# Optimization experiments

Measured on AMD Instinct MI355X. Metric: run time of the kernel, lower is better.

## Reference

```python
import jax, jax.numpy as jnp
import numpy as np

N_WAY, N_SHOT, C, H, W = 5, 5, 640, 32, 32
EPS = 1e-12


def conv1x1(x, w, b):
    # 1x1 conv == channel GEMM; w: (C_out, C_in), b: (C_out,)
    return jnp.einsum('bchw,oc->bohw', x, w) + b[None, :, None, None]


def setup_inputs() -> dict:
    key = jax.random.key(0)
    ks = jax.random.split(key, 7)
    B = N_WAY * N_SHOT
    x5 = jax.random.normal(ks[0], (B, C, H, W), jnp.float32)
    Wc = jax.random.normal(ks[1], (C, C), jnp.float32) * 0.02
    bc = jax.random.normal(ks[2], (C,), jnp.float32) * 0.02
    Wq = jax.random.normal(ks[3], (C, C), jnp.float32) * 0.02
    bq = jax.random.normal(ks[4], (C,), jnp.float32) * 0.02
    Wk = jax.random.normal(ks[5], (C, C), jnp.float32) * 0.02
    bk = jax.random.normal(ks[6], (C,), jnp.float32) * 0.02
    return {"x5": x5, "Wc": Wc, "bc": bc, "Wq": Wq, "bq": bq, "Wk": Wk, "bk": bk}


def reference(x5, Wc, bc, Wq, bq, Wk, bk):
    B, Cc, Hh, Ww = x5.shape
    HW = Hh * Ww
    scale = 1.0 / (Cc ** 0.5)

    # residual 1x1 conv, then query_transform applied once (x5 is reassigned)
    x5 = conv1x1(x5, Wc, bc) + x5
    x5 = conv1x1(x5, Wq, bq)

    # query: query_transform applied AGAIN on the already-transformed x5
    xq = conv1x1(x5, Wq, bq).reshape(N_WAY, N_SHOT, Cc, HW)
    xq = xq.transpose(0, 1, 3, 2).reshape(N_WAY, N_SHOT * HW, Cc)
    xk = conv1x1(x5, Wk, bk).reshape(N_WAY, N_SHOT, Cc, HW)
    xk = xk.transpose(0, 2, 1, 3).reshape(N_WAY, Cc, N_SHOT * HW)

    # QK scores per way: (n_way, S*HW, S*HW)
    xw = jnp.matmul(xq, xk) * scale
    # max over key spatial, mean over key shot
    xw = xw.reshape(N_WAY, N_SHOT * HW, N_SHOT, HW).max(-1).mean(-1)
    xw = jax.nn.softmax(xw.reshape(N_WAY, N_SHOT, HW), axis=-1)

    # channel-wise L2 normalize (F.normalize semantics)
    nrm = jnp.maximum(jnp.sqrt((x5 * x5).sum(1, keepdims=True)), EPS)
    norm0 = (x5 / nrm).reshape(N_WAY, N_SHOT, Cc, Hh, Ww)

    # argmax-equality mask over spatial positions
    xw_max = xw.max(-1, keepdims=True)
    mask = (xw == xw_max).astype(x5.dtype).reshape(N_WAY, N_SHOT, 1, Hh, Ww)

    # seeds: masked spatial sum of normalized features -> (n_way, n_shot, C)
    seeds = (norm0 * mask).sum((3, 4))

    # conv3d correlation: out[b,o,h,w] = sum_{k,c} norm0[b,k,c,h,w] * seeds[o,k,c]
    cm = jnp.einsum('bkchw,okc->bohw', norm0, seeds).reshape(N_WAY, N_WAY, HW)
    cmin = cm.min(-1, keepdims=True)
    cmax = cm.max(-1, keepdims=True)
    cm = (cm - cmin) / (cmax - cmin + EPS)
    cormap = cm.reshape(B, 1, Hh, Ww)

    x51 = (x5 * cormap).reshape(N_WAY, N_SHOT, Cc, Hh, Ww)
    proto1 = x51.mean((1, 3, 4))  # (n_way, C)
    return proto1
```

## Files before the change

kernel.cpp:

```cpp
#include <hip/hip_runtime.h>
#include <math.h>

#define NW 5
#define NS 5
#define CDIM 640
#define HWDIM 1024
#define BDIM 25
constexpr int CHW = CDIM * HWDIM;
constexpr int NBIG = BDIM * CHW;
constexpr int WSZ = CDIM * CDIM;
constexpr float QK_SCALE = 0.03952847075210474f;

typedef __attribute__((ext_vector_type(4))) float f32x4;
typedef __attribute__((ext_vector_type(8))) __bf16 bf16x8;
typedef __attribute__((ext_vector_type(4))) __bf16 bf16x4;
typedef __attribute__((ext_vector_type(2))) __bf16 bf16x2;

__device__ __forceinline__ void load_lds16(const __bf16* g, __bf16* l) {
    __builtin_amdgcn_global_load_lds(
        (const __attribute__((address_space(1))) void*)g,
        (__attribute__((address_space(3))) void*)l, 16, 0, 0);
}

__global__ __launch_bounds__(256) void split_f32(const float* __restrict__ s,
                                                 __bf16* __restrict__ dH,
                                                 __bf16* __restrict__ dL, int n4) {
    int i = blockIdx.x * 256 + threadIdx.x;
    if (i >= n4) return;
    f32x4 v = reinterpret_cast<const f32x4*>(s)[i];
    bf16x4 h, lo;
    #pragma unroll
    for (int q = 0; q < 4; ++q) {
        __bf16 hh = (__bf16)v[q];
        h[q] = hh;
        lo[q] = (__bf16)(v[q] - (float)hh);
    }
    reinterpret_cast<bf16x4*>(dH)[i] = h;
    reinterpret_cast<bf16x4*>(dL)[i] = lo;
}

__global__ __launch_bounds__(256) void tsplit(const float* __restrict__ x,
                                              __bf16* __restrict__ dH,
                                              __bf16* __restrict__ dL) {
    __shared__ float sT[32][33];
    const int hw0 = blockIdx.x * 32, c0 = blockIdx.y * 32, b = blockIdx.z;
    const int t = threadIdx.x;
    const int r = t >> 3, q4 = (t & 7) * 4;
    f32x4 v = *reinterpret_cast<const f32x4*>(
        &x[(size_t)b * CHW + (size_t)(c0 + r) * HWDIM + hw0 + q4]);
    #pragma unroll
    for (int i = 0; i < 4; ++i) sT[r][q4 + i] = v[i];
    __syncthreads();
    bf16x4 h, lo;
    #pragma unroll
    for (int i = 0; i < 4; ++i) {
        float xv = sT[q4 + i][r];
        __bf16 hh = (__bf16)xv;
        h[i] = hh;
        lo[i] = (__bf16)(xv - (float)hh);
    }
    size_t off = (size_t)b * CHW + (size_t)(hw0 + r) * CDIM + c0 + q4;
    *reinterpret_cast<bf16x4*>(&dH[off]) = h;
    *reinterpret_cast<bf16x4*>(&dL[off]) = lo;
}

template <int RES>
__global__ __launch_bounds__(256) void conv_mfma(
    const __bf16* __restrict__ inH, const __bf16* __restrict__ inL,
    const __bf16* __restrict__ wH, const __bf16* __restrict__ wL,
    const float* __restrict__ bias,
    __bf16* __restrict__ outH, __bf16* __restrict__ outL) {
    __shared__ __bf16 sA[2][128][32];
    __shared__ __bf16 sB[2][128][32];
    const int hw0 = blockIdx.x * 128;
    const int o0 = blockIdx.y * 128;
    const int b = blockIdx.z;
    const int tid = threadIdx.x;
    const int wv = tid >> 6, l = tid & 63;
    const int wo = (wv >> 1) * 64, wh = (wv & 1) * 64;
    const size_t inBase = (size_t)b * CHW;

    f32x4 acc[4][4];
    #pragma unroll
    for (int i = 0; i < 4; ++i)
        #pragma unroll
        for (int j = 0; j < 4; ++j) acc[i][j] = (f32x4){0.f, 0.f, 0.f, 0.f};

    const int srow = l >> 2;
    const int scol = (l & 3) * 8;
    const int fr = l & 15, fo = (l >> 4) * 8;

    for (int c0 = 0; c0 < CDIM; c0 += 32) {
        #pragma unroll
        for (int i = 0; i < 2; ++i) {
            const int r = wv * 32 + i * 16;
            const int gr = r + srow;
            load_lds16(&wH[(size_t)(o0 + gr) * CDIM + c0 + scol], &sA[0][r][0]);
            load_lds16(&wL[(size_t)(o0 + gr) * CDIM + c0 + scol], &sA[1][r][0]);
            load_lds16(&inH[inBase + (size_t)(hw0 + gr) * CDIM + c0 + scol],
                       &sB[0][r][0]);
            load_lds16(&inL[inBase + (size_t)(hw0 + gr) * CDIM + c0 + scol],
                       &sB[1][r][0]);
        }
        __syncthreads();
        bf16x8 aH[4], aL[4], bH[4], bL[4];
        #pragma unroll
        for (int i = 0; i < 4; ++i) {
            aH[i] = *reinterpret_cast<const bf16x8*>(&sA[0][wo + i * 16 + fr][fo]);
            aL[i] = *reinterpret_cast<const bf16x8*>(&sA[1][wo + i * 16 + fr][fo]);
            bH[i] = *reinterpret_cast<const bf16x8*>(&sB[0][wh + i * 16 + fr][fo]);
            bL[i] = *reinterpret_cast<const bf16x8*>(&sB[1][wh + i * 16 + fr][fo]);
        }
        #pragma unroll
        for (int i = 0; i < 4; ++i)
            #pragma unroll
            for (int j = 0; j < 4; ++j) {
                acc[i][j] = __builtin_amdgcn_mfma_f32_16x16x32_bf16(
                    aH[i], bH[j], acc[i][j], 0, 0, 0);
                acc[i][j] = __builtin_amdgcn_mfma_f32_16x16x32_bf16(
                    aH[i], bL[j], acc[i][j], 0, 0, 0);
                acc[i][j] = __builtin_amdgcn_mfma_f32_16x16x32_bf16(
                    aL[i], bH[j], acc[i][j], 0, 0, 0);
            }
        __syncthreads();
    }

    const int og = (l >> 4) * 4;
    const int cl = l & 15;
    #pragma unroll
    for (int i = 0; i < 4; ++i) {
        const int o = o0 + wo + i * 16 + og;
        const f32x4 bs = *reinterpret_cast<const f32x4*>(&bias[o]);
        #pragma unroll
        for (int j = 0; j < 4; ++j) {
            const int hw = hw0 + wh + j * 16 + cl;
            const size_t off = inBase + (size_t)hw * CDIM + o;
            float r[4];
            #pragma unroll
            for (int q = 0; q < 4; ++q) r[q] = acc[i][j][q] + bs[q];
            if (RES) {
                bf16x4 rh = *reinterpret_cast<const bf16x4*>(&inH[off]);
                bf16x4 rl = *reinterpret_cast<const bf16x4*>(&inL[off]);
                #pragma unroll
                for (int q = 0; q < 4; ++q) r[q] += (float)rh[q] + (float)rl[q];
            }
            bf16x4 oh, ol;
            #pragma unroll
            for (int q = 0; q < 4; ++q) {
                __bf16 hh = (__bf16)r[q];
                oh[q] = hh;
                ol[q] = (__bf16)(r[q] - (float)hh);
            }
            *reinterpret_cast<bf16x4*>(&outH[off]) = oh;
            *reinterpret_cast<bf16x4*>(&outL[off]) = ol;
        }
    }
}

__global__ __launch_bounds__(256) void attn_mfma(
    const __bf16* __restrict__ qH, const __bf16* __restrict__ qL,
    const __bf16* __restrict__ kH, const __bf16* __restrict__ kL,
    float* __restrict__ gpart) {
    __shared__ __bf16 sQ[2][128][32];
    __shared__ __bf16 sK[2][128][32];
    __shared__ float sRed[2][128];
    const int qt = blockIdx.x;
    const int ks = blockIdx.y, wy = blockIdx.z;
    const int sq = qt >> 3, q0 = (qt & 7) * 128;
    const int tid = threadIdx.x;
    const int wv = tid >> 6, l = tid & 63;
    const int wq = (wv >> 1) * 64;
    const int kh = wv & 1;
    const int wk = kh * 64;
    const size_t qBase = (size_t)(wy * NS + sq) * CHW;
    const size_t kBase = (size_t)(wy * NS + ks) * CHW;

    float qmax[4][4];
    #pragma unroll
    for (int i = 0; i < 4; ++i)
        #pragma unroll
        for (int q = 0; q < 4; ++q) qmax[i][q] = -INFINITY;

    const int srow = l >> 2, scol = (l & 3) * 8;
    const int fr = l & 15, fo = (l >> 4) * 8;

    for (int kc = 0; kc < HWDIM; kc += 128) {
        f32x4 acc[4][4];
        #pragma unroll
        for (int i = 0; i < 4; ++i)
            #pragma unroll
            for (int j = 0; j < 4; ++j) acc[i][j] = (f32x4){0.f, 0.f, 0.f, 0.f};

        for (int c0 = 0; c0 < CDIM; c0 += 32) {
            #pragma unroll
            for (int i = 0; i < 2; ++i) {
                const int r = wv * 32 + i * 16;
                const int gr = r + srow;
                load_lds16(&qH[qBase + (size_t)(q0 + gr) * CDIM + c0 + scol],
                           &sQ[0][r][0]);
                load_lds16(&qL[qBase + (size_t)(q0 + gr) * CDIM + c0 + scol],
                           &sQ[1][r][0]);
                load_lds16(&kH[kBase + (size_t)(kc + gr) * CDIM + c0 + scol],
                           &sK[0][r][0]);
                load_lds16(&kL[kBase + (size_t)(kc + gr) * CDIM + c0 + scol],
                           &sK[1][r][0]);
            }
            __syncthreads();
            bf16x8 aH[4], aL[4], bH[4], bL[4];
            #pragma unroll
            for (int i = 0; i < 4; ++i) {
                aH[i] = *reinterpret_cast<const bf16x8*>(&sQ[0][wq + i * 16 + fr][fo]);
                aL[i] = *reinterpret_cast<const bf16x8*>(&sQ[1][wq + i * 16 + fr][fo]);
                bH[i] = *reinterpret_cast<const bf16x8*>(&sK[0][wk + i * 16 + fr][fo]);
                bL[i] = *reinterpret_cast<const bf16x8*>(&sK[1][wk + i * 16 + fr][fo]);
            }
            #pragma unroll
            for (int i = 0; i < 4; ++i)
                #pragma unroll
                for (int j = 0; j < 4; ++j) {
                    acc[i][j] = __builtin_amdgcn_mfma_f32_16x16x32_bf16(
                        aH[i], bH[j], acc[i][j], 0, 0, 0);
                    acc[i][j] = __builtin_amdgcn_mfma_f32_16x16x32_bf16(
                        aH[i], bL[j], acc[i][j], 0, 0, 0);
                    acc[i][j] = __builtin_amdgcn_mfma_f32_16x16x32_bf16(
                        aL[i], bH[j], acc[i][j], 0, 0, 0);
                }
            __syncthreads();
        }
        #pragma unroll
        for (int i = 0; i < 4; ++i)
            #pragma unroll
            for (int q = 0; q < 4; ++q) {
                float m = fmaxf(fmaxf(acc[i][0][q], acc[i][1][q]),
                                fmaxf(acc[i][2][q], acc[i][3][q]));
                qmax[i][q] = fmaxf(qmax[i][q], m);
            }
    }
    #pragma unroll
    for (int i = 0; i < 4; ++i)
        #pragma unroll
        for (int q = 0; q < 4; ++q) {
            float v = qmax[i][q];
            v = fmaxf(v, __shfl_xor(v, 1));
            v = fmaxf(v, __shfl_xor(v, 2));
            v = fmaxf(v, __shfl_xor(v, 4));
            v = fmaxf(v, __shfl_xor(v, 8));
            qmax[i][q] = v;
        }
    if ((l & 15) == 0) {
        const int g = l >> 4;
        #pragma unroll
        for (int i = 0; i < 4; ++i)
            #pragma unroll
            for (int q = 0; q < 4; ++q)
                sRed[kh][wq + i * 16 + g * 4 + q] = qmax[i][q];
    }
    __syncthreads();
    if (tid < 128) {
        float m = fmaxf(sRed[0][tid], sRed[1][tid]);
        gpart[(size_t)(wy * NS + ks) * (NS * HWDIM) + sq * HWDIM + q0 + tid] =
            m * QK_SCALE;
    }
}

__global__ __launch_bounds__(256) void softmax_mask(const float* __restrict__ gpart,
                                                    int* __restrict__ gIdx,
                                                    int* __restrict__ gCnt) {
    const int bb = blockIdx.x;
    const int w = bb / NS, sq = bb % NS;
    const int tid = threadIdx.x;
    __shared__ float sred[256];
    __shared__ int sCnt;

    float v[4];
    #pragma unroll
    for (int i = 0; i < 4; ++i) {
        int hw = tid + 256 * i;
        float s = 0.f;
        #pragma unroll
        for (int ks = 0; ks < NS; ++ks)
            s += gpart[(size_t)(w * NS + ks) * (NS * HWDIM) + sq * HWDIM + hw];
        v[i] = s * 0.2f;
    }
    float m = fmaxf(fmaxf(v[0], v[1]), fmaxf(v[2], v[3]));
    sred[tid] = m;
    __syncthreads();
    for (int s = 128; s > 0; s >>= 1) {
        if (tid < s) sred[tid] = fmaxf(sred[tid], sred[tid + s]);
        __syncthreads();
    }
    float rowmax = sred[0];
    __syncthreads();
    float e[4], ls = 0.f;
    #pragma unroll
    for (int i = 0; i < 4; ++i) { e[i] = expf(v[i] - rowmax); ls += e[i]; }
    sred[tid] = ls;
    __syncthreads();
    for (int s = 128; s > 0; s >>= 1) {
        if (tid < s) sred[tid] += sred[tid + s];
        __syncthreads();
    }
    float ssum = sred[0];
    __syncthreads();
    float p[4], pm = 0.f;
    #pragma unroll
    for (int i = 0; i < 4; ++i) { p[i] = e[i] / ssum; pm = fmaxf(pm, p[i]); }
    sred[tid] = pm;
    __syncthreads();
    for (int s = 128; s > 0; s >>= 1) {
        if (tid < s) sred[tid] = fmaxf(sred[tid], sred[tid + s]);
        __syncthreads();
    }
    float pmax = sred[0];
    if (tid == 0) sCnt = 0;
    __syncthreads();
    #pragma unroll
    for (int i = 0; i < 4; ++i) {
        if (p[i] == pmax) {
            int slot = atomicAdd(&sCnt, 1);
            gIdx[bb * HWDIM + slot] = tid + 256 * i;
        }
    }
    __syncthreads();
    if (tid == 0) gCnt[bb] = sCnt;
}

__global__ __launch_bounds__(256) void nrm_k(const __bf16* __restrict__ yH,
                                             const __bf16* __restrict__ yL,
                                             float* __restrict__ inv) {
    const int row = blockIdx.x * 16 + (threadIdx.x >> 4);
    const int cq = threadIdx.x & 15;
    const size_t base = (size_t)row * CDIM;
    float s = 0.f;
    #pragma unroll
    for (int i = 0; i < 10; ++i) {
        int c = i * 64 + cq * 4;
        bf16x4 h = *reinterpret_cast<const bf16x4*>(&yH[base + c]);
        bf16x4 lo = *reinterpret_cast<const bf16x4*>(&yL[base + c]);
        #pragma unroll
        for (int q = 0; q < 4; ++q) {
            float x = (float)h[q] + (float)lo[q];
            s = fmaf(x, x, s);
        }
    }
    s += __shfl_xor(s, 1);
    s += __shfl_xor(s, 2);
    s += __shfl_xor(s, 4);
    s += __shfl_xor(s, 8);
    if (cq == 0) inv[row] = 1.0f / fmaxf(sqrtf(s), 1e-12f);
}

__global__ __launch_bounds__(640) void seeds_k(const __bf16* __restrict__ yH,
                                               const __bf16* __restrict__ yL,
                                               const float* __restrict__ inv,
                                               const int* __restrict__ gIdx,
                                               const int* __restrict__ gCnt,
                                               float* __restrict__ seeds) {
    const int bb = blockIdx.x, c = threadIdx.x;
    const int cnt = gCnt[bb];
    float s = 0.f;
    for (int e = 0; e < cnt; ++e) {
        int hw = gIdx[bb * HWDIM + e];
        size_t off = (size_t)bb * CHW + (size_t)hw * CDIM + c;
        s += ((float)yH[off] + (float)yL[off]) * inv[bb * HWDIM + hw];
    }
    seeds[bb * CDIM + c] = s;
}

__global__ __launch_bounds__(256) void cm_k(const __bf16* __restrict__ yH,
                                            const __bf16* __restrict__ yL,
                                            const float* __restrict__ inv,
                                            const float* __restrict__ seeds,
                                            float* __restrict__ cm) {
    __shared__ float sS[BDIM * CDIM];
    const int way = blockIdx.y;
    const int tid = threadIdx.x, wv = tid >> 6, l = tid & 63;
    const int hw = blockIdx.x * 4 + wv;
    for (int e = tid; e < BDIM * CDIM; e += 256) sS[e] = seeds[e];
    __syncthreads();
    float acc[NW] = {0.f, 0.f, 0.f, 0.f, 0.f};
    for (int k = 0; k < NS; ++k) {
        const size_t base = (size_t)(way * NS + k) * CHW + (size_t)hw * CDIM;
        float t[NW] = {0.f, 0.f, 0.f, 0.f, 0.f};
        #pragma unroll
        for (int i = 0; i < 5; ++i) {
            int c = (i * 64 + l) * 2;
            bf16x2 h = *reinterpret_cast<const bf16x2*>(&yH[base + c]);
            bf16x2 lo = *reinterpret_cast<const bf16x2*>(&yL[base + c]);
            float x0 = (float)h[0] + (float)lo[0];
            float x1 = (float)h[1] + (float)lo[1];
            #pragma unroll
            for (int o = 0; o < NW; ++o) {
                t[o] = fmaf(x0, sS[(o * NS + k) * CDIM + c], t[o]);
                t[o] = fmaf(x1, sS[(o * NS + k) * CDIM + c + 1], t[o]);
            }
        }
        float iv = inv[(way * NS + k) * HWDIM + hw];
        #pragma unroll
        for (int o = 0; o < NW; ++o) acc[o] = fmaf(t[o], iv, acc[o]);
    }
    #pragma unroll
    for (int o = 0; o < NW; ++o) {
        float v = acc[o];
        v += __shfl_xor(v, 1);
        v += __shfl_xor(v, 2);
        v += __shfl_xor(v, 4);
        v += __shfl_xor(v, 8);
        v += __shfl_xor(v, 16);
        v += __shfl_xor(v, 32);
        if (l == 0) cm[(size_t)(way * NW + o) * HWDIM + hw] = v;
    }
}

__global__ __launch_bounds__(256) void minmax_kernel(float* __restrict__ cm) {
    const int row = blockIdx.x;
    const int tid = threadIdx.x;
    __shared__ float smn[256], smx[256];
    float v[4];
    #pragma unroll
    for (int i = 0; i < 4; ++i) v[i] = cm[(size_t)row * HWDIM + tid + 256 * i];
    float mn = fminf(fminf(v[0], v[1]), fminf(v[2], v[3]));
    float mx = fmaxf(fmaxf(v[0], v[1]), fmaxf(v[2], v[3]));
    smn[tid] = mn;
    smx[tid] = mx;
    __syncthreads();
    for (int s = 128; s > 0; s >>= 1) {
        if (tid < s) {
            smn[tid] = fminf(smn[tid], smn[tid + s]);
            smx[tid] = fmaxf(smx[tid], smx[tid + s]);
        }
        __syncthreads();
    }
    float cmin = smn[0], cmax = smx[0];
    float den = cmax - cmin + 1e-12f;
    #pragma unroll
    for (int i = 0; i < 4; ++i)
        cm[(size_t)row * HWDIM + tid + 256 * i] = (v[i] - cmin) / den;
}

__global__ __launch_bounds__(128) void proto_part_k(const __bf16* __restrict__ yH,
                                                    const __bf16* __restrict__ yL,
                                                    const float* __restrict__ cmn,
                                                    float* __restrict__ part) {
    const int w = blockIdx.x, cc = blockIdx.y, hs = blockIdx.z;
    const int c = cc * 128 + threadIdx.x;
    float s = 0.f;
    for (int i = 0; i < 640; ++i) {
        int g = hs * 640 + i, sh = g >> 10, hw = g & 1023;
        size_t off = (size_t)(w * NS + sh) * CHW + (size_t)hw * CDIM + c;
        s = fmaf((float)yH[off] + (float)yL[off],
                 cmn[(w * NS + sh) * HWDIM + hw], s);
    }
    part[((w * 5 + cc) * 8 + hs) * 128 + threadIdx.x] = s;
}

__global__ __launch_bounds__(128) void proto_red_k(const float* __restrict__ part,
                                                   float* __restrict__ out) {
    const int bid = blockIdx.x;
    float s = 0.f;
    #pragma unroll
    for (int hs = 0; hs < 8; ++hs) s += part[(bid * 8 + hs) * 128 + threadIdx.x];
    const int w = bid / 5, cc = bid % 5;
    out[w * CDIM + cc * 128 + threadIdx.x] = s * (1.0f / 5120.0f);
}

extern "C" void kernel_launch(void* const* d_in, const int* in_sizes, int n_in,
                              void* d_out, int out_size, void* d_ws, size_t ws_size,
                              hipStream_t stream) {
    const float* x5 = (const float*)d_in[0];
    const float* Wc = (const float*)d_in[1];
    const float* bc = (const float*)d_in[2];
    const float* Wq = (const float*)d_in[3];
    const float* bq = (const float*)d_in[4];
    const float* Wk = (const float*)d_in[5];
    const float* bk = (const float*)d_in[6];
    float* out = (float*)d_out;

    __bf16* big = (__bf16*)d_ws;
    __bf16* A_hi = big;
    __bf16* A_lo = big + (size_t)NBIG;
    __bf16* B_hi = big + (size_t)2 * NBIG;
    __bf16* B_lo = big + (size_t)3 * NBIG;
    __bf16* C_hi = big + (size_t)4 * NBIG;
    __bf16* C_lo = big + (size_t)5 * NBIG;
    __bf16* wp = big + (size_t)6 * NBIG;
    __bf16* WcH = wp;
    __bf16* WcL = wp + WSZ;
    __bf16* WqH = wp + 2 * WSZ;
    __bf16* WqL = wp + 3 * WSZ;
    __bf16* WkH = wp + 4 * WSZ;
    __bf16* WkL = wp + 5 * WSZ;
    float* fp = (float*)(wp + 6 * WSZ);
    float* gpart = fp;
    float* invb = fp + 128000;
    float* seedsb = fp + 153600;
    float* cmb = fp + 169600;
    float* partb = fp + 195200;
    int* gIdx = (int*)(fp + 220800);
    int* gCnt = gIdx + BDIM * HWDIM;

    const int W4 = WSZ / 4;
    split_f32<<<dim3((W4 + 255) / 256), 256, 0, stream>>>(Wc, WcH, WcL, W4);
    split_f32<<<dim3((W4 + 255) / 256), 256, 0, stream>>>(Wq, WqH, WqL, W4);
    split_f32<<<dim3((W4 + 255) / 256), 256, 0, stream>>>(Wk, WkH, WkL, W4);
    tsplit<<<dim3(32, 20, 25), 256, 0, stream>>>(x5, A_hi, A_lo);

    dim3 gG(8, 5, 25);
    conv_mfma<1><<<gG, 256, 0, stream>>>(A_hi, A_lo, WcH, WcL, bc, B_hi, B_lo);
    conv_mfma<0><<<gG, 256, 0, stream>>>(B_hi, B_lo, WqH, WqL, bq, C_hi, C_lo);
    conv_mfma<0><<<gG, 256, 0, stream>>>(C_hi, C_lo, WqH, WqL, bq, B_hi, B_lo);
    conv_mfma<0><<<gG, 256, 0, stream>>>(C_hi, C_lo, WkH, WkL, bk, A_hi, A_lo);

    attn_mfma<<<dim3(40, 5, 5), 256, 0, stream>>>(B_hi, B_lo, A_hi, A_lo, gpart);
    softmax_mask<<<25, 256, 0, stream>>>(gpart, gIdx, gCnt);
    nrm_k<<<1600, 256, 0, stream>>>(C_hi, C_lo, invb);
    seeds_k<<<25, 640, 0, stream>>>(C_hi, C_lo, invb, gIdx, gCnt, seedsb);
    cm_k<<<dim3(256, 5), 256, 0, stream>>>(C_hi, C_lo, invb, seedsb, cmb);
    minmax_kernel<<<25, 256, 0, stream>>>(cmb);
    proto_part_k<<<dim3(5, 5, 8), 128, 0, stream>>>(C_hi, C_lo, cmb, partb);
    proto_red_k<<<25, 128, 0, stream>>>(partb, out);
}
```

Baseline: 1.072 ms.

## Interleave hi/lo bf16 tiles in XOR-swizzled LDS rows and raise MFMA priority

```diff
diff --git a/kernel.cpp b/kernel.cpp
--- a/kernel.cpp
+++ b/kernel.cpp
@@ -64,14 +64,29 @@
     *reinterpret_cast<bf16x4*>(&dL[off]) = lo;
 }
 
+
+__device__ __forceinline__ void stage_tile(const __bf16* __restrict__ srcH,
+                                           const __bf16* __restrict__ srcL,
+                                           __bf16* lds, int wv, int l, int c0) {
+    const int lch = (l & 7) ^ (l >> 3);
+    const int scol = (lch & 3) * 8;
+    const int srw = l >> 3;
+    const __bf16* src = (lch & 4) ? srcL : srcH;
+    #pragma unroll
+    for (int i = 0; i < 4; ++i) {
+        const int r0 = wv * 32 + i * 8;
+        load_lds16(&src[(size_t)(r0 + srw) * CDIM + c0 + scol], &lds[r0 * 64]);
+    }
+}
+
 template <int RES>
 __global__ __launch_bounds__(256) void conv_mfma(
     const __bf16* __restrict__ inH, const __bf16* __restrict__ inL,
     const __bf16* __restrict__ wH, const __bf16* __restrict__ wL,
     const float* __restrict__ bias,
     __bf16* __restrict__ outH, __bf16* __restrict__ outL) {
-    __shared__ __bf16 sA[2][128][32];
-    __shared__ __bf16 sB[2][128][32];
+    __shared__ __bf16 sA[128 * 64];
+    __shared__ __bf16 sB[128 * 64];
     const int hw0 = blockIdx.x * 128;
     const int o0 = blockIdx.y * 128;
     const int b = blockIdx.z;
@@ -80,36 +95,33 @@
     const int wo = (wv >> 1) * 64, wh = (wv & 1) * 64;
     const size_t inBase = (size_t)b * CHW;
 
+    const __bf16* wSrcH = wH + (size_t)o0 * CDIM;
+    const __bf16* wSrcL = wL + (size_t)o0 * CDIM;
+    const __bf16* iSrcH = inH + inBase + (size_t)hw0 * CDIM;
+    const __bf16* iSrcL = inL + inBase + (size_t)hw0 * CDIM;
+
     f32x4 acc[4][4];
     #pragma unroll
     for (int i = 0; i < 4; ++i)
         #pragma unroll
         for (int j = 0; j < 4; ++j) acc[i][j] = (f32x4){0.f, 0.f, 0.f, 0.f};
 
-    const int srow = l >> 2;
-    const int scol = (l & 3) * 8;
-    const int fr = l & 15, fo = (l >> 4) * 8;
+    const int fr = l & 15, cf = l >> 4;
+    const int ehi = (cf ^ (fr & 7)) * 8;
 
     for (int c0 = 0; c0 < CDIM; c0 += 32) {
-        #pragma unroll
-        for (int i = 0; i < 2; ++i) {
-            const int r = wv * 32 + i * 16;
-            const int gr = r + srow;
-            load_lds16(&wH[(size_t)(o0 + gr) * CDIM + c0 + scol], &sA[0][r][0]);
-            load_lds16(&wL[(size_t)(o0 + gr) * CDIM + c0 + scol], &sA[1][r][0]);
-            load_lds16(&inH[inBase + (size_t)(hw0 + gr) * CDIM + c0 + scol],
-                       &sB[0][r][0]);
-            load_lds16(&inL[inBase + (size_t)(hw0 + gr) * CDIM + c0 + scol],
-                       &sB[1][r][0]);
-        }
+        stage_tile(wSrcH, wSrcL, sA, wv, l, c0);
+        stage_tile(iSrcH, iSrcL, sB, wv, l, c0);
         __syncthreads();
         bf16x8 aH[4], aL[4], bH[4], bL[4];
         #pragma unroll
         for (int i = 0; i < 4; ++i) {
-            aH[i] = *reinterpret_cast<const bf16x8*>(&sA[0][wo + i * 16 + fr][fo]);
-            aL[i] = *reinterpret_cast<const bf16x8*>(&sA[1][wo + i * 16 + fr][fo]);
-            bH[i] = *reinterpret_cast<const bf16x8*>(&sB[0][wh + i * 16 + fr][fo]);
-            bL[i] = *reinterpret_cast<const bf16x8*>(&sB[1][wh + i * 16 + fr][fo]);
+            const int ra = (wo + i * 16 + fr) * 64;
+            const int rb = (wh + i * 16 + fr) * 64;
+            aH[i] = *reinterpret_cast<const bf16x8*>(&sA[ra + ehi]);
+            aL[i] = *reinterpret_cast<const bf16x8*>(&sA[ra + (ehi ^ 32)]);
+            bH[i] = *reinterpret_cast<const bf16x8*>(&sB[rb + ehi]);
+            bL[i] = *reinterpret_cast<const bf16x8*>(&sB[rb + (ehi ^ 32)]);
         }
         #pragma unroll
         for (int i = 0; i < 4; ++i)
@@ -161,8 +173,8 @@
     const __bf16* __restrict__ qH, const __bf16* __restrict__ qL,
     const __bf16* __restrict__ kH, const __bf16* __restrict__ kL,
     float* __restrict__ gpart) {
-    __shared__ __bf16 sQ[2][128][32];
-    __shared__ __bf16 sK[2][128][32];
+    __shared__ __bf16 sQ[128 * 64];
+    __shared__ __bf16 sK[128 * 64];
     __shared__ float sRed[2][128];
     const int qt = blockIdx.x;
     const int ks = blockIdx.y, wy = blockIdx.z;
@@ -172,8 +184,10 @@
     const int wq = (wv >> 1) * 64;
     const int kh = wv & 1;
     const int wk = kh * 64;
-    const size_t qBase = (size_t)(wy * NS + sq) * CHW;
-    const size_t kBase = (size_t)(wy * NS + ks) * CHW;
+    const __bf16* qSrcH = qH + (size_t)(wy * NS + sq) * CHW + (size_t)q0 * CDIM;
+    const __bf16* qSrcL = qL + (size_t)(wy * NS + sq) * CHW + (size_t)q0 * CDIM;
+    const __bf16* kBaseH = kH + (size_t)(wy * NS + ks) * CHW;
+    const __bf16* kBaseL = kL + (size_t)(wy * NS + ks) * CHW;
 
     float qmax[4][4];
     #pragma unroll
@@ -181,10 +195,12 @@
         #pragma unroll
         for (int q = 0; q < 4; ++q) qmax[i][q] = -INFINITY;
 
-    const int srow = l >> 2, scol = (l & 3) * 8;
-    const int fr = l & 15, fo = (l >> 4) * 8;
+    const int fr = l & 15, cf = l >> 4;
+    const int ehi = (cf ^ (fr & 7)) * 8;
 
     for (int kc = 0; kc < HWDIM; kc += 128) {
+        const __bf16* kSrcH = kBaseH + (size_t)kc * CDIM;
+        const __bf16* kSrcL = kBaseL + (size_t)kc * CDIM;
         f32x4 acc[4][4];
         #pragma unroll
         for (int i = 0; i < 4; ++i)
@@ -192,28 +208,20 @@
             for (int j = 0; j < 4; ++j) acc[i][j] = (f32x4){0.f, 0.f, 0.f, 0.f};
 
         for (int c0 = 0; c0 < CDIM; c0 += 32) {
-            #pragma unroll
-            for (int i = 0; i < 2; ++i) {
-                const int r = wv * 32 + i * 16;
-                const int gr = r + srow;
-                load_lds16(&qH[qBase + (size_t)(q0 + gr) * CDIM + c0 + scol],
-                           &sQ[0][r][0]);
-                load_lds16(&qL[qBase + (size_t)(q0 + gr) * CDIM + c0 + scol],
-                           &sQ[1][r][0]);
-                load_lds16(&kH[kBase + (size_t)(kc + gr) * CDIM + c0 + scol],
-                           &sK[0][r][0]);
-                load_lds16(&kL[kBase + (size_t)(kc + gr) * CDIM + c0 + scol],
-                           &sK[1][r][0]);
-            }
+            stage_tile(qSrcH, qSrcL, sQ, wv, l, c0);
+            stage_tile(kSrcH, kSrcL, sK, wv, l, c0);
             __syncthreads();
             bf16x8 aH[4], aL[4], bH[4], bL[4];
             #pragma unroll
             for (int i = 0; i < 4; ++i) {
-                aH[i] = *reinterpret_cast<const bf16x8*>(&sQ[0][wq + i * 16 + fr][fo]);
-                aL[i] = *reinterpret_cast<const bf16x8*>(&sQ[1][wq + i * 16 + fr][fo]);
-                bH[i] = *reinterpret_cast<const bf16x8*>(&sK[0][wk + i * 16 + fr][fo]);
-                bL[i] = *reinterpret_cast<const bf16x8*>(&sK[1][wk + i * 16 + fr][fo]);
+                const int ra = (wq + i * 16 + fr) * 64;
+                const int rb = (wk + i * 16 + fr) * 64;
+                aH[i] = *reinterpret_cast<const bf16x8*>(&sQ[ra + ehi]);
+                aL[i] = *reinterpret_cast<const bf16x8*>(&sQ[ra + (ehi ^ 32)]);
+                bH[i] = *reinterpret_cast<const bf16x8*>(&sK[rb + ehi]);
+                bL[i] = *reinterpret_cast<const bf16x8*>(&sK[rb + (ehi ^ 32)]);
             }
+            __builtin_amdgcn_s_setprio(1);
             #pragma unroll
             for (int i = 0; i < 4; ++i)
                 #pragma unroll
@@ -225,6 +233,7 @@
                     acc[i][j] = __builtin_amdgcn_mfma_f32_16x16x32_bf16(
                         aL[i], bH[j], acc[i][j], 0, 0, 0);
                 }
+            __builtin_amdgcn_s_setprio(0);
             __syncthreads();
         }
         #pragma unroll
```

Result: no change. 1.084 ms (+1.1%).
